# Optimization experiments

Hardware: AMD Instinct MI355X
Metric: run time of the kernel (lower is better)

The kernel has to match this reference:

```python
import jax, jax.numpy as jnp
import numpy as np

D_MODEL = 1024
NUM_HEAD = 16
D_K = D_MODEL // NUM_HEAD


def setup_inputs() -> dict:
    key = jax.random.key(0)
    ks = jax.random.split(key, 9)
    s = 1.0 / np.sqrt(D_MODEL)
    x = jax.random.normal(ks[0], (2, 2048, D_MODEL), dtype=jnp.float32)
    Wq = jax.random.uniform(ks[1], (D_MODEL, D_MODEL), jnp.float32, -s, s)
    bq = jax.random.uniform(ks[2], (D_MODEL,), jnp.float32, -s, s)
    Wk = jax.random.uniform(ks[3], (D_MODEL, D_MODEL), jnp.float32, -s, s)
    bk = jax.random.uniform(ks[4], (D_MODEL,), jnp.float32, -s, s)
    Wv = jax.random.uniform(ks[5], (D_MODEL, D_MODEL), jnp.float32, -s, s)
    bv = jax.random.uniform(ks[6], (D_MODEL,), jnp.float32, -s, s)
    Wo = jax.random.uniform(ks[7], (D_MODEL, D_MODEL), jnp.float32, -s, s)
    bo = jax.random.uniform(ks[8], (D_MODEL,), jnp.float32, -s, s)
    return {"x": x, "Wq": Wq, "bq": bq, "Wk": Wk, "bk": bk,
            "Wv": Wv, "bv": bv, "Wo": Wo, "bo": bo}


def reference(x, Wq, bq, Wk, bk, Wv, bv, Wo, bo):
    b, n, d = x.shape
    h, dk = NUM_HEAD, D_K
    # Linear projections (torch Linear: x @ W.T + b)
    q = (x @ Wq.T + bq).reshape(b, n, h, dk).transpose(0, 2, 1, 3)  # [b,h,n,dk]
    k = (x @ Wk.T + bk).reshape(b, n, h, dk).transpose(0, 2, 1, 3)
    v = (x @ Wv.T + bv).reshape(b, n, h, dk).transpose(0, 2, 1, 3)
    scores = jnp.einsum('bhqd,bhkd->bhqk', q, k) / jnp.sqrt(jnp.float32(dk))
    attn = jax.nn.softmax(scores, axis=-1)  # [b,h,n,n]
    out = jnp.einsum('bhqk,bhkd->bhqd', attn, v)
    out = out.transpose(0, 2, 1, 3).reshape(b, n, d)
    return out @ Wo.T + bo
```

## Files before the change

kernel.cpp:

```cpp
#include <hip/hip_runtime.h>

#define BATCH   2
#define SEQ     2048
#define DMODEL  1024
#define NHEAD   16
#define DKH     64
#define MTOT    (BATCH*SEQ)
#define KDIM    DMODEL

#define XB    0u
#define WQB   (4u*1024u*1024u)
#define WKB   (5u*1024u*1024u)
#define WVB   (6u*1024u*1024u)
#define WOB   (7u*1024u*1024u)
#define QOFF  (8u*1024u*1024u)
#define KOFF  (12u*1024u*1024u)
#define VOFF  (16u*1024u*1024u)
#define OOFF  (20u*1024u*1024u)

typedef __bf16 bf16x8 __attribute__((ext_vector_type(8)));
typedef __bf16 bf16x4 __attribute__((ext_vector_type(4)));
typedef float  f32x4  __attribute__((ext_vector_type(4)));
typedef float  f32x16 __attribute__((ext_vector_type(16)));

__device__ __forceinline__ void async16(const __bf16* g, __bf16* l) {
  __builtin_amdgcn_global_load_lds(
      (const __attribute__((address_space(1))) void*)g,
      (__attribute__((address_space(3))) void*)l, 16, 0, 0);
}

__device__ __forceinline__ unsigned cvtpk_bf16(float lo, float hi) {
  unsigned r;
  asm("v_cvt_pk_bf16_f32 %0, %1, %2" : "=v"(r) : "v"(lo), "v"(hi));
  return r;
}
__device__ __forceinline__ void plswap(unsigned& a, unsigned& b) {
  asm("v_permlane32_swap_b32 %0, %1" : "+v"(a), "+v"(b));
}

__global__ __launch_bounds__(256) void cvt_fp32_bf16(
    const float* __restrict__ x,  const float* __restrict__ wq,
    const float* __restrict__ wk, const float* __restrict__ wv,
    const float* __restrict__ wo, __bf16* __restrict__ ws)
{
  const float* src; __bf16* dst; int n;
  switch (blockIdx.y) {
    case 0:  src = x;  dst = ws + XB;  n = 4 * 1024 * 1024; break;
    case 1:  src = wq; dst = ws + WQB; n = 1024 * 1024;     break;
    case 2:  src = wk; dst = ws + WKB; n = 1024 * 1024;     break;
    case 3:  src = wv; dst = ws + WVB; n = 1024 * 1024;     break;
    default: src = wo; dst = ws + WOB; n = 1024 * 1024;     break;
  }
  const int i = (blockIdx.x * 256 + threadIdx.x) * 8;
  if (i < n) {
    const float4 a = *(const float4*)(src + i);
    const float4 b = *(const float4*)(src + i + 4);
    bf16x8 o;
    o[0] = (__bf16)a.x; o[1] = (__bf16)a.y; o[2] = (__bf16)a.z; o[3] = (__bf16)a.w;
    o[4] = (__bf16)b.x; o[5] = (__bf16)b.y; o[6] = (__bf16)b.z; o[7] = (__bf16)b.w;
    *(bf16x8*)(dst + i) = o;
  }
}

__device__ __forceinline__ void gemm128_core(
    const __bf16* __restrict__ A, const __bf16* __restrict__ W,
    int m0, int n0, __bf16* lds, f32x4 (&acc)[4][4])
{
  __bf16* A_lds = lds;
  __bf16* B_lds = lds + 4096;
  const int t    = threadIdx.x;
  const int w    = t >> 6;
  const int lane = t & 63;
  const int ln15 = lane & 15;
  const int quad = lane >> 4;
  const int wr   = (w >> 1) << 6;
  const int wc   = (w & 1) << 6;

#pragma unroll
  for (int i = 0; i < 4; ++i)
#pragma unroll
    for (int j = 0; j < 4; ++j) acc[i][j] = (f32x4){0.f, 0.f, 0.f, 0.f};

  for (int kt = 0; kt < KDIM; kt += 32) {
    __syncthreads();
#pragma unroll
    for (int issue = 0; issue < 2; ++issue) {
      const int cbase = issue * 256 + (w << 6);
      const int c     = cbase + lane;
      const int row   = c >> 2;
      const int goff  = ((c & 3) ^ (row & 3)) << 3;
      async16(A + (size_t)(m0 + row) * KDIM + kt + goff, A_lds + cbase * 8);
      async16(W + (size_t)(n0 + row) * KDIM + kt + goff, B_lds + cbase * 8);
    }
    __syncthreads();

    bf16x8 af[4], bfr[4];
#pragma unroll
    for (int i = 0; i < 4; ++i) {
      const int row = wr + i * 16 + ln15;
      af[i] = *(const bf16x8*)&A_lds[row * 32 + ((quad ^ (row & 3)) << 3)];
    }
#pragma unroll
    for (int j = 0; j < 4; ++j) {
      const int row = wc + j * 16 + ln15;
      bfr[j] = *(const bf16x8*)&B_lds[row * 32 + ((quad ^ (row & 3)) << 3)];
    }
#pragma unroll
    for (int i = 0; i < 4; ++i)
#pragma unroll
      for (int j = 0; j < 4; ++j)
        acc[i][j] = __builtin_amdgcn_mfma_f32_16x16x32_bf16(af[i], bfr[j], acc[i][j], 0, 0, 0);
  }
}

__global__ __launch_bounds__(256) void qkv_gemm(
    const __bf16* __restrict__ X,
    const __bf16* __restrict__ Wq, const float* __restrict__ bq,
    const __bf16* __restrict__ Wk, const float* __restrict__ bk,
    const __bf16* __restrict__ Wv, const float* __restrict__ bv,
    __bf16* __restrict__ ws)
{
  __shared__ __align__(16) __bf16 lds[128 * 64];

  const int z = blockIdx.z;
  const __bf16* W    = (z == 0) ? Wq : (z == 1) ? Wk : Wv;
  const float*  bias = (z == 0) ? bq : (z == 1) ? bk : bv;
  __bf16* out = ws + ((z == 0) ? QOFF : (z == 1) ? KOFF : VOFF);
  const float scale = (z == 0) ? 0.125f * 1.44269504088896f : 1.0f;

  const int m0 = blockIdx.x * 128;
  const int n0 = blockIdx.y * 128;

  f32x4 acc[4][4];
  gemm128_core(X, W, m0, n0, lds, acc);

  const int t = threadIdx.x, w = t >> 6, lane = t & 63;
  const int ln15 = lane & 15, quad = lane >> 4;
  const int wr = (w >> 1) << 6, wc = (w & 1) << 6;

  float bj4[4];
#pragma unroll
  for (int j = 0; j < 4; ++j) bj4[j] = bias[n0 + wc + j * 16 + ln15];

  __syncthreads();
  __bf16* scr = lds + (w << 10);

  const int bb = m0 >> 11;
  const int s_base = (m0 & 2047) + wr;
  const int h = (n0 + wc) >> 6;

  if (z != 2) {
    const int rdrow = lane & 15, rdseg = lane >> 4;
#pragma unroll
    for (int i = 0; i < 4; ++i) {
#pragma unroll
      for (int j = 0; j < 4; ++j)
#pragma unroll
        for (int rr = 0; rr < 4; ++rr)
          scr[(quad * 4 + rr) * 64 + j * 16 + ln15] =
              (__bf16)((acc[i][j][rr] + bj4[j]) * scale);
      bf16x8 v0 = *(const bf16x8*)&scr[rdrow * 64 + rdseg * 16];
      bf16x8 v1 = *(const bf16x8*)&scr[rdrow * 64 + rdseg * 16 + 8];
      const int s = s_base + i * 16 + rdrow;
      __bf16* p = out + (((size_t)(bb * NHEAD + h)) * SEQ + s) * DKH + rdseg * 16;
      *(bf16x8*)p = v0;
      *(bf16x8*)&p[8] = v1;
    }
  } else {
#pragma unroll
    for (int i = 0; i < 4; ++i) {
#pragma unroll
      for (int j = 0; j < 4; ++j) {
        bf16x4 pk;
#pragma unroll
        for (int rr = 0; rr < 4; ++rr) pk[rr] = (__bf16)(acc[i][j][rr] + bj4[j]);
        *(bf16x4*)&scr[(j * 16 + ln15) * 16 + quad * 4] = pk;
      }
      bf16x8 c0 = *(const bf16x8*)&scr[lane * 16];
      bf16x8 c1 = *(const bf16x8*)&scr[lane * 16 + 8];
      __bf16* p = out + (((size_t)(bb * NHEAD + h)) * DKH + lane) * SEQ
                      + s_base + i * 16;
      *(bf16x8*)p = c0;
      *(bf16x8*)&p[8] = c1;
    }
  }
}

__global__ __launch_bounds__(256) void out_gemm(
    const __bf16* __restrict__ A, const __bf16* __restrict__ Wo,
    const float* __restrict__ bo, float* __restrict__ out)
{
  __shared__ __align__(16) __bf16 lds[6144];
  __bf16* A_lds = lds;
  __bf16* B_lds = lds + 2048;

  const int m0 = blockIdx.x * 64;
  const int n0 = blockIdx.y * 128;

  const int t = threadIdx.x, w = t >> 6, lane = t & 63;
  const int ln15 = lane & 15, quad = lane >> 4;

  f32x4 acc[4][2];
#pragma unroll
  for (int i = 0; i < 4; ++i)
#pragma unroll
    for (int j = 0; j < 2; ++j) acc[i][j] = (f32x4){0.f, 0.f, 0.f, 0.f};

  for (int kt = 0; kt < KDIM; kt += 32) {
    __syncthreads();
    {
      const int c = (w << 6) + lane;
      const int row = c >> 2;
      const int goff = ((c & 3) ^ (row & 3)) << 3;
      async16(A + (size_t)(m0 + row) * KDIM + kt + goff, A_lds + c * 8);
    }
#pragma unroll
    for (int issue = 0; issue < 2; ++issue) {
      const int cbase = issue * 256 + (w << 6);
      const int c = cbase + lane;
      const int row = c >> 2;
      const int goff = ((c & 3) ^ (row & 3)) << 3;
      async16(Wo + (size_t)(n0 + row) * KDIM + kt + goff, B_lds + cbase * 8);
    }
    __syncthreads();

    bf16x8 af[4], bfr[2];
#pragma unroll
    for (int i = 0; i < 4; ++i) {
      const int row = i * 16 + ln15;
      af[i] = *(const bf16x8*)&A_lds[row * 32 + ((quad ^ (row & 3)) << 3)];
    }
#pragma unroll
    for (int j = 0; j < 2; ++j) {
      const int row = (w << 5) + j * 16 + ln15;
      bfr[j] = *(const bf16x8*)&B_lds[row * 32 + ((quad ^ (row & 3)) << 3)];
    }
#pragma unroll
    for (int i = 0; i < 4; ++i)
#pragma unroll
      for (int j = 0; j < 2; ++j)
        acc[i][j] = __builtin_amdgcn_mfma_f32_16x16x32_bf16(af[i], bfr[j], acc[i][j], 0, 0, 0);
  }

  float bj2[2];
#pragma unroll
  for (int j = 0; j < 2; ++j) bj2[j] = bo[n0 + (w << 5) + j * 16 + ln15];

  __syncthreads();
  float* scrf = (float*)lds + (w << 9);

  const int rdrow = lane & 15, rdseg = lane >> 4;
#pragma unroll
  for (int i = 0; i < 4; ++i) {
#pragma unroll
    for (int j = 0; j < 2; ++j) {
      f32x4 v;
#pragma unroll
      for (int rr = 0; rr < 4; ++rr) v[rr] = acc[i][j][rr] + bj2[j];
      *(f32x4*)&scrf[(j * 16 + ln15) * 16 + quad * 4] = v;
    }
    const int m = m0 + i * 16 + rdrow;
    float* p = out + (size_t)m * DMODEL + n0 + (w << 5) + rdseg * 8;
#pragma unroll
    for (int cc = 0; cc < 2; ++cc) {
      f32x4 v;
#pragma unroll
      for (int e = 0; e < 4; ++e)
        v[e] = scrf[(rdseg * 8 + cc * 4 + e) * 16 + rdrow];
      *(f32x4*)&p[cc * 4] = v;
    }
  }
}

__device__ __forceinline__ void softmax_frag(const f32x16& s, float& l,
                                             bf16x8& pfa, bf16x8& pfb)
{
  float p[16];
#pragma unroll
  for (int r = 0; r < 16; ++r) {
    p[r] = __builtin_amdgcn_exp2f(s[r]);
    l += p[r];
  }
  unsigned A0 = cvtpk_bf16(p[0],  p[1]);
  unsigned A1 = cvtpk_bf16(p[2],  p[3]);
  unsigned B0 = cvtpk_bf16(p[4],  p[5]);
  unsigned B1 = cvtpk_bf16(p[6],  p[7]);
  unsigned C0 = cvtpk_bf16(p[8],  p[9]);
  unsigned C1 = cvtpk_bf16(p[10], p[11]);
  unsigned D0 = cvtpk_bf16(p[12], p[13]);
  unsigned D1 = cvtpk_bf16(p[14], p[15]);
  plswap(A0, B0);
  plswap(A1, B1);
  plswap(C0, D0);
  plswap(C1, D1);
  union { unsigned u[4]; bf16x8 v; } ua, ub;
  ua.u[0] = A0; ua.u[1] = A1; ua.u[2] = B0; ua.u[3] = B1;
  ub.u[0] = C0; ub.u[1] = C1; ub.u[2] = D0; ub.u[3] = D1;
  pfa = ua.v;
  pfb = ub.v;
}

__device__ __forceinline__ void pvstep(const __bf16* Vs, int kh, int KS, int hl,
                                       int ln31, const bf16x8& PF,
                                       f32x16& o0, f32x16& o1)
{
  const int vchunk = (kh << 3) + 2 * KS + hl;
  bf16x8 vf0 = *(const bf16x8*)&Vs[ln31 * 128 + ((vchunk ^ (ln31 & 15)) << 3)];
  bf16x8 vf1 = *(const bf16x8*)&Vs[(32 + ln31) * 128 +
                                   ((vchunk ^ ((32 + ln31) & 15)) << 3)];
  o0 = __builtin_amdgcn_mfma_f32_32x32x16_bf16(PF, vf0, o0, 0, 0, 0);
  o1 = __builtin_amdgcn_mfma_f32_32x32x16_bf16(PF, vf1, o1, 0, 0, 0);
}

__device__ __forceinline__ void attn_tile_compute(
    const __bf16* Ks, const __bf16* Vs, const bf16x8 (&qf)[4],
    int kh, int ln31, int hl, float& l_lane, f32x16& o0, f32x16& o1)
{
  f32x16 s0, s1;
#pragma unroll
  for (int r = 0; r < 16; ++r) { s0[r] = 0.f; s1[r] = 0.f; }
  const int kr0 = (kh << 6) + ln31;
  const int kr1 = (kh << 6) + 32 + ln31;

  __builtin_amdgcn_s_setprio(1);
#pragma unroll
  for (int ks = 0; ks < 4; ++ks) {
    bf16x8 kf0 = *(const bf16x8*)&Ks[kr0 * 64 + (((2 * ks + hl) ^ (kr0 & 7)) << 3)];
    bf16x8 kf1 = *(const bf16x8*)&Ks[kr1 * 64 + (((2 * ks + hl) ^ (kr1 & 7)) << 3)];
    s0 = __builtin_amdgcn_mfma_f32_32x32x16_bf16(kf0, qf[ks], s0, 0, 0, 0);
    s1 = __builtin_amdgcn_mfma_f32_32x32x16_bf16(kf1, qf[ks], s1, 0, 0, 0);
  }
  __builtin_amdgcn_s_setprio(0);

  bf16x8 pa0, pb0;
  softmax_frag(s0, l_lane, pa0, pb0);
  __builtin_amdgcn_s_setprio(1);
  pvstep(Vs, kh, 0, hl, ln31, pa0, o0, o1);
  pvstep(Vs, kh, 1, hl, ln31, pb0, o0, o1);
  __builtin_amdgcn_s_setprio(0);

  bf16x8 pa1, pb1;
  softmax_frag(s1, l_lane, pa1, pb1);
  __builtin_amdgcn_s_setprio(1);
  pvstep(Vs, kh, 2, hl, ln31, pa1, o0, o1);
  pvstep(Vs, kh, 3, hl, ln31, pb1, o0, o1);
  __builtin_amdgcn_s_setprio(0);
}

__global__ __launch_bounds__(512, 4) void attn_kernel(
    const __bf16* __restrict__ Qb, const __bf16* __restrict__ Kb,
    const __bf16* __restrict__ Vtb, __bf16* __restrict__ Ob)
{
  __shared__ __align__(16) __bf16 smem[3 * 128 * 64];
  __bf16* QP = smem;
  __bf16* Ks = smem + 8192;
  __bf16* Vs = smem + 16384;

  const int t = threadIdx.x, w = t >> 6, lane = t & 63;
  const int ln31 = lane & 31, hl = lane >> 5;
  const int g  = w & 3;
  const int kh = w >> 2;
  const int bh = blockIdx.x;
  const int q0 = blockIdx.y * 128;
  const int bb = bh >> 4, hh = bh & 15;

  const __bf16* Qg = Qb + (size_t)bh * SEQ * DKH + (size_t)q0 * DKH;
  const __bf16* Kg = Kb + (size_t)bh * SEQ * DKH;
  const __bf16* Vg = Vtb + (size_t)bh * DKH * SEQ;

#pragma unroll
  for (int issue = 0; issue < 2; ++issue) {
    const int cbase = issue * 512 + (w << 6);
    const int c = cbase + lane;
    const int row = c >> 3;
    const int goff = ((c & 7) ^ (row & 7)) << 3;
    async16(Qg + (size_t)row * DKH + goff, QP + cbase * 8);
  }
  __syncthreads();

  const int qrow = (g << 5) + ln31;
  bf16x8 qf[4];
#pragma unroll
  for (int ks = 0; ks < 4; ++ks) {
    const int chunk = ((2 * ks + hl) ^ (qrow & 7));
    qf[ks] = *(const bf16x8*)&QP[qrow * 64 + (chunk << 3)];
  }

  float l_lane = 0.f;
  f32x16 o0, o1;
#pragma unroll
  for (int r = 0; r < 16; ++r) { o0[r] = 0.f; o1[r] = 0.f; }

  for (int kt = 0; kt < SEQ; kt += 128) {
    __syncthreads();
#pragma unroll
    for (int issue = 0; issue < 2; ++issue) {
      const int cbase = issue * 512 + (w << 6);
      const int c = cbase + lane;
      const int krow = c >> 3;
      const int kgoff = ((c & 7) ^ (krow & 7)) << 3;
      async16(Kg + (size_t)(kt + krow) * DKH + kgoff, Ks + cbase * 8);
      const int vrow = c >> 4;
      const int vgoff = ((c & 15) ^ (vrow & 15)) << 3;
      async16(Vg + (size_t)vrow * SEQ + kt + vgoff, Vs + cbase * 8);
    }
    __syncthreads();

    attn_tile_compute(Ks, Vs, qf, kh, ln31, hl, l_lane, o0, o1);
  }

  __syncthreads();
  float* cmb = (float*)smem;
  const int dsw = ln31 & 7;
  l_lane += __shfl_xor(l_lane, 32);

  if (w >= 4) {
    float* base = cmb + (g << 11);
#pragma unroll
    for (int gg = 0; gg < 4; ++gg) {
      const int qq = ((2 * gg + hl) ^ dsw) << 2;
      f32x4 va, vb;
#pragma unroll
      for (int rr = 0; rr < 4; ++rr) { va[rr] = o0[4 * gg + rr]; vb[rr] = o1[4 * gg + rr]; }
      *(f32x4*)&base[ln31 * 32 + qq]        = va;
      *(f32x4*)&base[(32 + ln31) * 32 + qq] = vb;
    }
    if (hl == 0) cmb[8192 + (g << 5) + ln31] = l_lane;
  }
  __syncthreads();
  if (w < 4) {
    float* base = cmb + (g << 11);
#pragma unroll
    for (int gg = 0; gg < 4; ++gg) {
      const int qq = ((2 * gg + hl) ^ dsw) << 2;
      const f32x4 va = *(const f32x4*)&base[ln31 * 32 + qq];
      const f32x4 vb = *(const f32x4*)&base[(32 + ln31) * 32 + qq];
#pragma unroll
      for (int rr = 0; rr < 4; ++rr) { o0[4 * gg + rr] += va[rr]; o1[4 * gg + rr] += vb[rr]; }
    }
    const float inv = 1.0f / (l_lane + cmb[8192 + (g << 5) + ln31]);

#pragma unroll
    for (int r = 0; r < 16; ++r) {
      const int qi = (r & 3) + 8 * (r >> 2) + 4 * hl;
      const float iq = __shfl(inv, qi);
      const int q = q0 + (g << 5) + qi;
      __bf16* rowp = Ob + ((size_t)(bb * SEQ + q)) * DMODEL + hh * DKH;
      rowp[ln31]      = (__bf16)(o0[r] * iq);
      rowp[32 + ln31] = (__bf16)(o1[r] * iq);
    }
  }
}

extern "C" void kernel_launch(void* const* d_in, const int* in_sizes, int n_in,
                              void* d_out, int out_size, void* d_ws, size_t ws_size,
                              hipStream_t stream)
{
  const float* x  = (const float*)d_in[0];
  const float* Wq = (const float*)d_in[1];
  const float* bq = (const float*)d_in[2];
  const float* Wk = (const float*)d_in[3];
  const float* bk = (const float*)d_in[4];
  const float* Wv = (const float*)d_in[5];
  const float* bv = (const float*)d_in[6];
  const float* Wo = (const float*)d_in[7];
  const float* bo = (const float*)d_in[8];
  float*  out = (float*)d_out;
  __bf16* ws  = (__bf16*)d_ws;

  cvt_fp32_bf16<<<dim3(2048, 5, 1), 256, 0, stream>>>(x, Wq, Wk, Wv, Wo, ws);

  qkv_gemm<<<dim3(MTOT / 128, DMODEL / 128, 3), 256, 0, stream>>>(
      ws + XB, ws + WQB, bq, ws + WKB, bk, ws + WVB, bv, ws);

  attn_kernel<<<dim3(BATCH * NHEAD, SEQ / 128), 512, 0, stream>>>(
      ws + QOFF, ws + KOFF, ws + VOFF, ws + OOFF);

  out_gemm<<<dim3(MTOT / 64, DMODEL / 128), 256, 0, stream>>>(
      ws + OOFF, ws + WOB, bo, out);
}
```

Baseline: 190.3 us.

## Load two 128-key K/V tiles per barrier pair in attention loop

The attention main loop now stages two 128-key K and V sub-tiles into shared memory per iteration and runs two tile computes between each pair of barriers. This halves the number of block-wide synchronisations and gives the memory system larger batches of async loads in flight. The tile compute is also rewritten as a loop over key halves, so only one score accumulator is live at a time, which may lower register pressure. Shared memory grows from 48 KB to 80 KB per block, which can reduce how many blocks fit on a CU.

```diff
diff --git a/kernel.cpp b/kernel.cpp
--- a/kernel.cpp
+++ b/kernel.cpp
@@ -316,45 +316,36 @@
     const __bf16* Ks, const __bf16* Vs, const bf16x8 (&qf)[4],
     int kh, int ln31, int hl, float& l_lane, f32x16& o0, f32x16& o1)
 {
-  f32x16 s0, s1;
-#pragma unroll
-  for (int r = 0; r < 16; ++r) { s0[r] = 0.f; s1[r] = 0.f; }
-  const int kr0 = (kh << 6) + ln31;
-  const int kr1 = (kh << 6) + 32 + ln31;
-
-  __builtin_amdgcn_s_setprio(1);
-#pragma unroll
-  for (int ks = 0; ks < 4; ++ks) {
-    bf16x8 kf0 = *(const bf16x8*)&Ks[kr0 * 64 + (((2 * ks + hl) ^ (kr0 & 7)) << 3)];
-    bf16x8 kf1 = *(const bf16x8*)&Ks[kr1 * 64 + (((2 * ks + hl) ^ (kr1 & 7)) << 3)];
-    s0 = __builtin_amdgcn_mfma_f32_32x32x16_bf16(kf0, qf[ks], s0, 0, 0, 0);
-    s1 = __builtin_amdgcn_mfma_f32_32x32x16_bf16(kf1, qf[ks], s1, 0, 0, 0);
-  }
-  __builtin_amdgcn_s_setprio(0);
-
-  bf16x8 pa0, pb0;
-  softmax_frag(s0, l_lane, pa0, pb0);
-  __builtin_amdgcn_s_setprio(1);
-  pvstep(Vs, kh, 0, hl, ln31, pa0, o0, o1);
-  pvstep(Vs, kh, 1, hl, ln31, pb0, o0, o1);
-  __builtin_amdgcn_s_setprio(0);
-
-  bf16x8 pa1, pb1;
-  softmax_frag(s1, l_lane, pa1, pb1);
-  __builtin_amdgcn_s_setprio(1);
-  pvstep(Vs, kh, 2, hl, ln31, pa1, o0, o1);
-  pvstep(Vs, kh, 3, hl, ln31, pb1, o0, o1);
-  __builtin_amdgcn_s_setprio(0);
+#pragma unroll
+  for (int half = 0; half < 2; ++half) {
+    f32x16 s;
+#pragma unroll
+    for (int r = 0; r < 16; ++r) s[r] = 0.f;
+    const int kr = (kh << 6) + half * 32 + ln31;
+    __builtin_amdgcn_s_setprio(1);
+#pragma unroll
+    for (int ks = 0; ks < 4; ++ks) {
+      bf16x8 kf = *(const bf16x8*)&Ks[kr * 64 + (((2 * ks + hl) ^ (kr & 7)) << 3)];
+      s = __builtin_amdgcn_mfma_f32_32x32x16_bf16(kf, qf[ks], s, 0, 0, 0);
+    }
+    __builtin_amdgcn_s_setprio(0);
+    bf16x8 pa, pb;
+    softmax_frag(s, l_lane, pa, pb);
+    __builtin_amdgcn_s_setprio(1);
+    pvstep(Vs, kh, half * 2 + 0, hl, ln31, pa, o0, o1);
+    pvstep(Vs, kh, half * 2 + 1, hl, ln31, pb, o0, o1);
+    __builtin_amdgcn_s_setprio(0);
+  }
 }
 
 __global__ __launch_bounds__(512, 4) void attn_kernel(
     const __bf16* __restrict__ Qb, const __bf16* __restrict__ Kb,
     const __bf16* __restrict__ Vtb, __bf16* __restrict__ Ob)
 {
-  __shared__ __align__(16) __bf16 smem[3 * 128 * 64];
+  __shared__ __align__(16) __bf16 smem[5 * 128 * 64];
   __bf16* QP = smem;
   __bf16* Ks = smem + 8192;
-  __bf16* Vs = smem + 16384;
+  __bf16* Vs = smem + 24576;
 
   const int t = threadIdx.x, w = t >> 6, lane = t & 63;
   const int ln31 = lane & 31, hl = lane >> 5;
@@ -391,22 +382,29 @@
 #pragma unroll
   for (int r = 0; r < 16; ++r) { o0[r] = 0.f; o1[r] = 0.f; }
 
-  for (int kt = 0; kt < SEQ; kt += 128) {
-    __syncthreads();
-#pragma unroll
-    for (int issue = 0; issue < 2; ++issue) {
-      const int cbase = issue * 512 + (w << 6);
-      const int c = cbase + lane;
-      const int krow = c >> 3;
-      const int kgoff = ((c & 7) ^ (krow & 7)) << 3;
-      async16(Kg + (size_t)(kt + krow) * DKH + kgoff, Ks + cbase * 8);
-      const int vrow = c >> 4;
-      const int vgoff = ((c & 15) ^ (vrow & 15)) << 3;
-      async16(Vg + (size_t)vrow * SEQ + kt + vgoff, Vs + cbase * 8);
-    }
-    __syncthreads();
-
-    attn_tile_compute(Ks, Vs, qf, kh, ln31, hl, l_lane, o0, o1);
+  for (int kt = 0; kt < SEQ; kt += 256) {
+    __syncthreads();
+#pragma unroll
+    for (int sub = 0; sub < 2; ++sub) {
+      __bf16* Kd = Ks + sub * 8192;
+      __bf16* Vd = Vs + sub * 8192;
+      const int ktе_base = kt + sub * 128;
+#pragma unroll
+      for (int issue = 0; issue < 2; ++issue) {
+        const int cbase = issue * 512 + (w << 6);
+        const int c = cbase + lane;
+        const int krow = c >> 3;
+        const int kgoff = ((c & 7) ^ (krow & 7)) << 3;
+        async16(Kg + (size_t)(ktе_base + krow) * DKH + kgoff, Kd + cbase * 8);
+        const int vrow = c >> 4;
+        const int vgoff = ((c & 15) ^ (vrow & 15)) << 3;
+        async16(Vg + (size_t)vrow * SEQ + ktе_base + vgoff, Vd + cbase * 8);
+      }
+    }
+    __syncthreads();
+
+    attn_tile_compute(Ks,        Vs,        qf, kh, ln31, hl, l_lane, o0, o1);
+    attn_tile_compute(Ks + 8192, Vs + 8192, qf, kh, ln31, hl, l_lane, o0, o1);
   }
 
   __syncthreads();
```

New measurement: 186.4 us. 2.0% less time.
